# Optimization experiments

Hardware: AMD Instinct MI355X
Metric: run time of the kernel (lower is better)

## Reference

```python
import jax, jax.numpy as jnp
import numpy as np

CLASSES = 100
SIGMA = 1.0
K_MIX = 11   # mixup pseudo-label kNN
K_KNN = 3    # knn regularizer


def _pairwise_sq(a, b):
    # ||a_i - b_j||^2 via Gram trick; a:[M,D], b:[N,D] -> [M,N]
    aa = jnp.sum(a * a, axis=1)[:, None]
    bb = jnp.sum(b * b, axis=1)[None, :]
    return aa + bb - 2.0 * (a @ b.T)


def _mode_rows(vals):
    # vals: [M,K] float labels. torch.mode semantics: most frequent value,
    # smallest value on ties.
    eq = vals[:, :, None] == vals[:, None, :]      # [M,K,K]
    counts = jnp.sum(eq.astype(vals.dtype), axis=2)  # [M,K]
    maxc = jnp.max(counts, axis=1, keepdims=True)
    masked = jnp.where(counts == maxc, vals, jnp.inf)
    return jnp.min(masked, axis=1)


def setup_inputs() -> dict:
    key = jax.random.key(0)
    k1, k2, k3, k4 = jax.random.split(key, 4)
    N, D = 4096, 512
    x = jax.random.normal(k1, (N, D), dtype=jnp.float32)
    y = jax.random.randint(k2, (N,), 0, CLASSES).astype(jnp.float32)
    lam = jax.random.beta(k3, 2.0, 2.0, (), dtype=jnp.float32)  # Beta(alpha=2, alpha=2)
    perm = jax.random.permutation(k4, N).astype(jnp.int32)
    return {"x": x, "y": y, "lam": lam, "perm": perm}


def reference(x, y, lam, perm):
    # ---- mixup branch: pseudo-label mixed samples via k=11 NN mode ----
    x_ul = x * lam + x[perm] * (1.0 - lam)              # [N,D]
    d = _pairwise_sq(x_ul, x)                            # [N,N]
    _, idx = jax.lax.top_k(-d, K_MIX)                    # indices of k smallest dists
    y_ul = _mode_rows(y[idx])                            # [N]
    x = jnp.concatenate([x, x_ul], axis=0)               # [2N,D]
    y = jnp.concatenate([y, y_ul], axis=0)               # [2N]

    num = x.shape[0]
    y_int = y.astype(jnp.int32)
    # per-class means (empty classes masked out, as the torch loop skips them)
    counts = jax.ops.segment_sum(jnp.ones((num,), x.dtype), y_int, num_segments=CLASSES)
    mu = jax.ops.segment_sum(x, y_int, num_segments=CLASSES) / jnp.maximum(counts, 1.0)[:, None]
    d2 = _pairwise_sq(x, mu)                             # [num, classes]
    pi = jnp.exp(-d2 / (2.0 * SIGMA ** 2)) * (counts > 0).astype(x.dtype)[None, :]
    yh = jax.nn.one_hot(y_int, CLASSES, dtype=x.dtype)
    eps = 1e-15
    pi = pi / (jnp.sum(pi, axis=1, keepdims=True) + eps)
    pi = jnp.clip(pi, 0.0, 1.0)
    loss_gm = jnp.mean(jnp.sum((pi - yh) ** 2, axis=1))

    # ---- knn regularizer: k=3 NN (excluding self) mode label, MSE ----
    dk = _pairwise_sq(x, x)                              # [num,num]
    _, idxk = jax.lax.top_k(-dk, K_KNN + 1)              # nearest is self (dist 0)
    y_ng = _mode_rows(y[idxk[:, 1:]])
    loss_knn = jnp.mean((y_ng - y) ** 2)
    return loss_gm + 0.01 * loss_knn
```

## Files before the change

### kernel.cpp

```cpp
#include <hip/hip_runtime.h>
#include <math.h>

#define N0   4096
#define D    512
#define NUM  8192
#define NCLS 100
#define KMIX 11

#define OFF_NALL   0
#define OFF_YALL   8192
#define OFF_RLOSS  16384
#define OFF_KSQ    24576
#define OFF_MUSUM  32768
#define OFF_CNT    83968
#define OFF_KNN    84096
#define ZERO_N     51344
#define OFF_NMU    84112
#define OFF_MUT    84224
#define OFF_TK1S   135424
#define OFF_TK1I   659712
#define OFF_TK2S   1184000
#define OFF_TK2I   1446144
#define OFF_XH     1708288
#define TOTAL_F    3805440
#define NEED_BYTES ((size_t)TOTAL_F * 4)

typedef _Float16 half8 __attribute__((ext_vector_type(8)));
typedef _Float16 half4v __attribute__((ext_vector_type(4)));
typedef float f32x4 __attribute__((ext_vector_type(4)));
typedef unsigned long long u64;

__device__ __forceinline__ float4 ld_row4(const float* __restrict__ x, const int* __restrict__ perm,
                                          float lam, float om, int r, int col) {
  if (r < N0) {
    return *(const float4*)(x + (size_t)r * D + col);
  } else {
    int rr = r - N0;
    int p = perm[rr];
    float4 a = *(const float4*)(x + (size_t)rr * D + col);
    float4 b = *(const float4*)(x + (size_t)p * D + col);
    float4 m;
    m.x = lam * a.x + om * b.x;  m.y = lam * a.y + om * b.y;
    m.z = lam * a.z + om * b.z;  m.w = lam * a.w + om * b.w;
    return m;
  }
}

__device__ __forceinline__ void gld_lds16(const _Float16* g, _Float16* l) {
  __builtin_amdgcn_global_load_lds(
      (const __attribute__((address_space(1))) void*)g,
      (__attribute__((address_space(3))) void*)l, 16, 0, 0);
}

__device__ __forceinline__ unsigned sortable(float s) {
  unsigned u = __float_as_uint(s);
  return ((int)u < 0) ? ~u : (u | 0x80000000u);
}
__device__ __forceinline__ float unsortable(unsigned u) {
  return __uint_as_float(((int)u < 0) ? (u & 0x7fffffffu) : ~u);
}

__global__ __launch_bounds__(256) void k_zero(float* __restrict__ p, int n) {
  int i = blockIdx.x * 256 + threadIdx.x;
  if (i < n) p[i] = 0.f;
}

__global__ __launch_bounds__(256) void k_y(const float* __restrict__ y, float* __restrict__ y_all) {
  int i = blockIdx.x * 256 + threadIdx.x;
  if (i < N0) y_all[i] = y[i];
}

__global__ __launch_bounds__(64) void k_prep(const float* __restrict__ x, const float* __restrict__ y,
                                             const int* __restrict__ perm, const float* __restrict__ lam_p,
                                             _Float16* __restrict__ Xh, float* __restrict__ n_all,
                                             float* __restrict__ y_all) {
  int i = blockIdx.x;
  float lam = lam_p[0], om = 1.0f - lam;
  int t = threadIdx.x;
  float4 a = ld_row4(x, perm, lam, om, i, t * 4);
  float4 b = ld_row4(x, perm, lam, om, i, t * 4 + 256);
  half4v ha, hb;
  ha.x = (_Float16)a.x; ha.y = (_Float16)a.y; ha.z = (_Float16)a.z; ha.w = (_Float16)a.w;
  hb.x = (_Float16)b.x; hb.y = (_Float16)b.y; hb.z = (_Float16)b.z; hb.w = (_Float16)b.w;
  *(half4v*)(Xh + (size_t)i * D + t * 4) = ha;
  *(half4v*)(Xh + (size_t)i * D + t * 4 + 256) = hb;
  float s = a.x*a.x + a.y*a.y + a.z*a.z + a.w*a.w
          + b.x*b.x + b.y*b.y + b.z*b.z + b.w*b.w;
  #pragma unroll
  for (int o = 32; o > 0; o >>= 1) s += __shfl_down(s, o, 64);
  if (t == 0) {
    n_all[i] = s;
    if (i < N0) y_all[i] = y[i];
  }
}

template<int M, int NSPL>
__device__ __forceinline__ void knn_body(const _Float16* __restrict__ Xq,
                                         const _Float16* __restrict__ Xc,
                                         const float* __restrict__ nC,
                                         int cb0, int candPerSplit,
                                         int row0, int split,
                                         float* __restrict__ outS, int* __restrict__ outI,
                                         char* smem) {
  float* Ss = (float*)smem;
  _Float16* St = (_Float16*)smem;
  u64* Lb = (u64*)smem;

  int tid = threadIdx.x;
  int wave = tid >> 6, lane = tid & 63;
  int wq = wave >> 1, wc = wave & 1;
  int col16 = lane & 15, quad = lane >> 4;

  const _Float16* qg = Xq + (size_t)(wave * 16 + col16) * D + quad * 8;
  int csegA = 2 * wave, csegB = 2 * wave + 1;
  int ldsQ = wave * 1024 + lane * 8;
  int ldsCA = 4096 + csegA * 1024 + lane * 8;
  int ldsCB = 4096 + csegB * 1024 + lane * 8;

  u64 keys[M];
  #pragma unroll
  for (int q = 0; q < M; q++) keys[q] = ~0ULL;

  int r_scan = tid & 63, h_scan = tid >> 6;

  for (int c0 = 0; c0 < candPerSplit; c0 += 128) {
    const _Float16* cgA = Xc + (size_t)(cb0 + c0 + csegA * 16 + col16) * D + quad * 8;
    const _Float16* cgB = cgA + (size_t)16 * D;

    f32x4 acc[2][4];
    #pragma unroll
    for (int i = 0; i < 2; i++)
      #pragma unroll
      for (int j = 0; j < 4; j++) acc[i][j] = (f32x4){0.f, 0.f, 0.f, 0.f};

    gld_lds16(qg,       St + ldsQ);
    gld_lds16(qg + 32,  St + ldsQ + 512);
    gld_lds16(cgA,      St + ldsCA);
    gld_lds16(cgA + 32, St + ldsCA + 512);
    gld_lds16(cgB,      St + ldsCB);
    gld_lds16(cgB + 32, St + ldsCB + 512);
    __syncthreads();

    #pragma unroll
    for (int t = 0; t < 8; t++) {
      const int cur = t & 1;
      if (t < 7) {
        int kk = (t + 1) * 64;
        _Float16* B = St + (cur ^ 1) * 12288;
        gld_lds16(qg + kk,       B + ldsQ);
        gld_lds16(qg + kk + 32,  B + ldsQ + 512);
        gld_lds16(cgA + kk,      B + ldsCA);
        gld_lds16(cgA + kk + 32, B + ldsCA + 512);
        gld_lds16(cgB + kk,      B + ldsCB);
        gld_lds16(cgB + kk + 32, B + ldsCB + 512);
      }
      const _Float16* Bc = St + cur * 12288;
      half8 a[2][2], b[4][2];
      #pragma unroll
      for (int i = 0; i < 2; i++)
        #pragma unroll
        for (int h = 0; h < 2; h++)
          a[i][h] = *(const half8*)(Bc + (wq * 2 + i) * 1024 + h * 512 + lane * 8);
      #pragma unroll
      for (int j = 0; j < 4; j++)
        #pragma unroll
        for (int h = 0; h < 2; h++)
          b[j][h] = *(const half8*)(Bc + 4096 + (wc * 4 + j) * 1024 + h * 512 + lane * 8);
      #pragma unroll
      for (int h = 0; h < 2; h++)
        #pragma unroll
        for (int i = 0; i < 2; i++)
          #pragma unroll
          for (int j = 0; j < 4; j++)
            acc[i][j] = __builtin_amdgcn_mfma_f32_16x16x32_f16(a[i][h], b[j][h], acc[i][j], 0, 0, 0);
      __syncthreads();
    }

    #pragma unroll
    for (int j = 0; j < 4; j++) {
      int c_local = wc * 64 + j * 16 + col16;
      float ncv = nC[cb0 + c0 + c_local];
      #pragma unroll
      for (int i = 0; i < 2; i++) {
        float4 st;
        st.x = ncv - 2.f * acc[i][j][0];
        st.y = ncv - 2.f * acc[i][j][1];
        st.z = ncv - 2.f * acc[i][j][2];
        st.w = ncv - 2.f * acc[i][j][3];
        *(float4*)&Ss[(size_t)c_local * 68 + wq * 32 + i * 16 + quad * 4] = st;
      }
    }
    __syncthreads();

    for (int c = h_scan * 32; c < h_scan * 32 + 32; c++) {
      float s = Ss[c * 68 + r_scan];
      u64 key = ((u64)sortable(s) << 32) | (unsigned)(cb0 + c0 + c);
      if (key < keys[M - 1]) {
        keys[M - 1] = key;
        #pragma unroll
        for (int p = M - 1; p > 0; p--) {
          if (keys[p] < keys[p - 1]) { u64 tmp = keys[p]; keys[p] = keys[p - 1]; keys[p - 1] = tmp; }
        }
      }
    }
    __syncthreads();
  }

  #pragma unroll
  for (int q = 0; q < M; q++)
    Lb[((size_t)h_scan * 64 + r_scan) * M + q] = keys[q];
  __syncthreads();
  if (tid < 64) {
    int p0 = 0, p1 = 0, p2 = 0, p3 = 0;
    const u64* L0 = Lb + (size_t)(0 * 64 + tid) * M;
    const u64* L1 = Lb + (size_t)(1 * 64 + tid) * M;
    const u64* L2 = Lb + (size_t)(2 * 64 + tid) * M;
    const u64* L3 = Lb + (size_t)(3 * 64 + tid) * M;
    size_t off = (size_t)(row0 + tid) * ((size_t)NSPL * M) + (size_t)split * M;
    #pragma unroll
    for (int q = 0; q < M; q++) {
      u64 k0 = (p0 < M) ? L0[p0] : ~0ULL;
      u64 k1 = (p1 < M) ? L1[p1] : ~0ULL;
      u64 k2 = (p2 < M) ? L2[p2] : ~0ULL;
      u64 k3 = (p3 < M) ? L3[p3] : ~0ULL;
      u64 b01 = k0 < k1 ? k0 : k1;
      u64 b23 = k2 < k3 ? k2 : k3;
      u64 b = b01 < b23 ? b01 : b23;
      if (b == k0) p0++; else if (b == k1) p1++; else if (b == k2) p2++; else p3++;
      outS[off + q] = unsortable((unsigned)(b >> 32));
      outI[off + q] = (int)(unsigned)b;
    }
  }
}

__global__ __launch_bounds__(256, 3) void k_knn_all(const _Float16* __restrict__ Xh,
                                                    const float* __restrict__ n_all,
                                                    float* __restrict__ tk1s, int* __restrict__ tk1i,
                                                    float* __restrict__ tk2s, int* __restrict__ tk2i) {
  __shared__ __align__(16) char smem[49152];
  int bx = blockIdx.x;
  if (bx < 512) {
    int qblk = bx & 127, split = bx >> 7;
    knn_body<8, 4>(Xh + (size_t)(qblk * 64) * D, Xh, n_all,
                   split * 2048, 2048, qblk * 64, split, tk2s, tk2i, smem);
  } else {
    int b = bx - 512;
    int qblk = b & 63, split = b >> 6;
    knn_body<16, 8>(Xh + (size_t)(N0 + qblk * 64) * D, Xh, n_all,
                    split * 512, 512, qblk * 64, split, tk1s, tk1i, smem);
  }
}

__global__ __launch_bounds__(256) void k_rr1(const float* __restrict__ x, const int* __restrict__ perm,
                                             const float* __restrict__ lam_p,
                                             const float* __restrict__ tks, const int* __restrict__ tki,
                                             const float* __restrict__ n_all, const float* __restrict__ y,
                                             float* __restrict__ y_all) {
  __shared__ int sidx[16];
  __shared__ float sdot[16];
  int i = blockIdx.x;
  int t = threadIdx.x;
  float lam = lam_p[0], om = 1.f - lam;
  if (t == 0) {
    const float* sb = tks + (size_t)i * 128;
    const int* ib = tki + (size_t)i * 128;
    int p[8] = {0,0,0,0,0,0,0,0};
    for (int q = 0; q < 16; q++) {
      float bs = 3.0e38f; int bi = 0x7fffffff; int w = 0;
      #pragma unroll
      for (int li = 0; li < 8; li++) {
        if (p[li] < 16) {
          float s = sb[li * 16 + p[li]]; int id = ib[li * 16 + p[li]];
          if (s < bs || (s == bs && id < bi)) { bs = s; bi = id; w = li; }
        }
      }
      p[w]++;
      sidx[q] = bi;
    }
  }
  __syncthreads();
  int g = t >> 4, l16 = t & 15;
  int c = sidx[g];
  float dot = 0.f;
  for (int d0 = l16 * 4; d0 < D; d0 += 64) {
    float4 q4 = ld_row4(x, perm, lam, om, N0 + i, d0);
    float4 c4 = *(const float4*)(x + (size_t)c * D + d0);
    dot += q4.x*c4.x + q4.y*c4.y + q4.z*c4.z + q4.w*c4.w;
  }
  #pragma unroll
  for (int o = 8; o > 0; o >>= 1) dot += __shfl_down(dot, o, 16);
  if (l16 == 0) sdot[g] = n_all[c] - 2.f * dot;
  __syncthreads();
  if (t == 0) {
    float es[16]; int ei[16];
    for (int q = 0; q < 16; q++) { es[q] = sdot[q]; ei[q] = sidx[q]; }
    for (int a = 1; a < 16; a++) {
      float s = es[a]; int id = ei[a];
      int b = a - 1;
      while (b >= 0 && (es[b] > s || (es[b] == s && ei[b] > id))) {
        es[b + 1] = es[b]; ei[b + 1] = ei[b]; b--;
      }
      es[b + 1] = s; ei[b + 1] = id;
    }
    float lab[KMIX];
    for (int q = 0; q < KMIX; q++) lab[q] = y[ei[q]];
    float best = 3.0e38f; int bestc = 0;
    for (int q = 0; q < KMIX; q++) {
      int cnt = 0;
      for (int r = 0; r < KMIX; r++) cnt += (lab[r] == lab[q]) ? 1 : 0;
      if (cnt > bestc || (cnt == bestc && lab[q] < best)) { bestc = cnt; best = lab[q]; }
    }
    y_all[N0 + i] = best;
  }
}

__global__ __launch_bounds__(256) void k_rr2(const float* __restrict__ x, const int* __restrict__ perm,
                                             const float* __restrict__ lam_p,
                                             const float* __restrict__ tks, const int* __restrict__ tki,
                                             const float* __restrict__ n_all, const float* __restrict__ y_all,
                                             float* __restrict__ ksq) {
  __shared__ int sidx[8];
  __shared__ float sdot[8];
  int i = blockIdx.x;
  int t = threadIdx.x;
  float lam = lam_p[0], om = 1.f - lam;
  if (t == 0) {
    const float* sb = tks + (size_t)i * 32;
    const int* ib = tki + (size_t)i * 32;
    int p[4] = {0,0,0,0};
    for (int q = 0; q < 8; q++) {
      float bs = 3.0e38f; int bi = 0x7fffffff; int w = 0;
      #pragma unroll
      for (int li = 0; li < 4; li++) {
        if (p[li] < 8) {
          float s = sb[li * 8 + p[li]]; int id = ib[li * 8 + p[li]];
          if (s < bs || (s == bs && id < bi)) { bs = s; bi = id; w = li; }
        }
      }
      p[w]++;
      sidx[q] = bi;
    }
  }
  __syncthreads();
  int g = t >> 5, l32 = t & 31;
  int c = sidx[g];
  float dot = 0.f;
  for (int d0 = l32 * 4; d0 < D; d0 += 128) {
    float4 q4 = ld_row4(x, perm, lam, om, i, d0);
    float4 c4 = ld_row4(x, perm, lam, om, c, d0);
    dot += q4.x*c4.x + q4.y*c4.y + q4.z*c4.z + q4.w*c4.w;
  }
  #pragma unroll
  for (int o = 16; o > 0; o >>= 1) dot += __shfl_down(dot, o, 32);
  if (l32 == 0) sdot[g] = n_all[c] - 2.f * dot;
  __syncthreads();
  if (t == 0) {
    float es[8]; int ei[8];
    for (int q = 0; q < 8; q++) { es[q] = sdot[q]; ei[q] = sidx[q]; }
    for (int a = 1; a < 8; a++) {
      float s = es[a]; int id = ei[a];
      int b = a - 1;
      while (b >= 0 && (es[b] > s || (es[b] == s && ei[b] > id))) {
        es[b + 1] = es[b]; ei[b + 1] = ei[b]; b--;
      }
      es[b + 1] = s; ei[b + 1] = id;
    }
    float l1 = y_all[ei[1]], l2 = y_all[ei[2]], l3 = y_all[ei[3]];
    int c1 = 1 + (int)(l2 == l1) + (int)(l3 == l1);
    int c2 = 1 + (int)(l1 == l2) + (int)(l3 == l2);
    int c3 = 1 + (int)(l1 == l3) + (int)(l2 == l3);
    int mc = c1 > c2 ? c1 : c2; mc = mc > c3 ? mc : c3;
    float mv = 3.0e38f;
    if (c1 == mc) mv = fminf(mv, l1);
    if (c2 == mc) mv = fminf(mv, l2);
    if (c3 == mc) mv = fminf(mv, l3);
    float d = mv - y_all[i];
    ksq[i] = d * d;
  }
}

__global__ __launch_bounds__(256) void k_stats2h(const float* __restrict__ x, const int* __restrict__ perm,
                                                 const float* __restrict__ lam_p, const float* __restrict__ y_all,
                                                 _Float16* __restrict__ muH, float* __restrict__ nmu_pad,
                                                 float* __restrict__ counts) {
  __shared__ int cnt;
  __shared__ int lst[NUM];
  __shared__ int lstp[NUM];
  __shared__ float red[256];
  int c = blockIdx.x;
  int t = threadIdx.x;
  if (c >= NCLS) {
    for (int d = t; d < D; d += 256) muH[(size_t)c * D + d] = (_Float16)0.f;
    if (t == 0) { nmu_pad[c] = 0.f; counts[c] = 0.f; }
    return;
  }
  float lam = lam_p[0], om = 1.f - lam;
  float fc = (float)c;
  if (t == 0) cnt = 0;
  __syncthreads();
  for (int i = t; i < NUM; i += 256) {
    if (y_all[i] == fc) {
      int pos = atomicAdd(&cnt, 1);
      lst[pos] = i;
      lstp[pos] = (i >= N0) ? perm[i - N0] : 0;
    }
  }
  __syncthreads();
  int n = cnt;
  float a0 = 0.f, a1 = 0.f;
  for (int m = 0; m < n; m++) {
    int i = lst[m];
    if (i < N0) {
      a0 += x[(size_t)i * D + t];
      a1 += x[(size_t)i * D + t + 256];
    } else {
      int rr = i - N0, p = lstp[m];
      a0 += lam * x[(size_t)rr * D + t] + om * x[(size_t)p * D + t];
      a1 += lam * x[(size_t)rr * D + t + 256] + om * x[(size_t)p * D + t + 256];
    }
  }
  float inv = 1.f / fmaxf((float)n, 1.f);
  float v0 = a0 * inv, v1 = a1 * inv;
  muH[(size_t)c * D + t] = (_Float16)v0;
  muH[(size_t)c * D + t + 256] = (_Float16)v1;
  red[t] = v0 * v0 + v1 * v1;
  __syncthreads();
  for (int o = 128; o > 0; o >>= 1) { if (t < o) red[t] += red[t + o]; __syncthreads(); }
  if (t == 0) { nmu_pad[c] = red[0]; counts[c] = (float)n; }
}

__global__ __launch_bounds__(256) void k_gm2(const _Float16* __restrict__ Xh,
                                             const _Float16* __restrict__ muH,
                                             const float* __restrict__ nmu_pad,
                                             const float* __restrict__ counts,
                                             const float* __restrict__ n_all,
                                             const float* __restrict__ y_all,
                                             float* __restrict__ rloss) {
  __shared__ __align__(16) char smem[49152];
  float* Ss = (float*)smem;
  _Float16* St = (_Float16*)smem;

  int tid = threadIdx.x;
  int wave = tid >> 6, lane = tid & 63;
  int wq = wave >> 1, wc = wave & 1;
  int col16 = lane & 15, quad = lane >> 4;
  int qb = blockIdx.x * 64;

  const _Float16* qg = Xh + (size_t)(qb + wave * 16 + col16) * D + quad * 8;
  int csegA = 2 * wave, csegB = 2 * wave + 1;
  const _Float16* cgA = muH + (size_t)(csegA * 16 + col16) * D + quad * 8;
  const _Float16* cgB = cgA + (size_t)16 * D;
  int ldsQ = wave * 1024 + lane * 8;
  int ldsCA = 4096 + csegA * 1024 + lane * 8;
  int ldsCB = 4096 + csegB * 1024 + lane * 8;

  f32x4 acc[2][4];
  #pragma unroll
  for (int i = 0; i < 2; i++)
    #pragma unroll
    for (int j = 0; j < 4; j++) acc[i][j] = (f32x4){0.f, 0.f, 0.f, 0.f};

  gld_lds16(qg,       St + ldsQ);
  gld_lds16(qg + 32,  St + ldsQ + 512);
  gld_lds16(cgA,      St + ldsCA);
  gld_lds16(cgA + 32, St + ldsCA + 512);
  gld_lds16(cgB,      St + ldsCB);
  gld_lds16(cgB + 32, St + ldsCB + 512);
  __syncthreads();

  #pragma unroll
  for (int t = 0; t < 8; t++) {
    const int cur = t & 1;
    if (t < 7) {
      int kk = (t + 1) * 64;
      _Float16* B = St + (cur ^ 1) * 12288;
      gld_lds16(qg + kk,       B + ldsQ);
      gld_lds16(qg + kk + 32,  B + ldsQ + 512);
      gld_lds16(cgA + kk,      B + ldsCA);
      gld_lds16(cgA + kk + 32, B + ldsCA + 512);
      gld_lds16(cgB + kk,      B + ldsCB);
      gld_lds16(cgB + kk + 32, B + ldsCB + 512);
    }
    const _Float16* Bc = St + cur * 12288;
    half8 a[2][2], b[4][2];
    #pragma unroll
    for (int i = 0; i < 2; i++)
      #pragma unroll
      for (int h = 0; h < 2; h++)
        a[i][h] = *(const half8*)(Bc + (wq * 2 + i) * 1024 + h * 512 + lane * 8);
    #pragma unroll
    for (int j = 0; j < 4; j++)
      #pragma unroll
      for (int h = 0; h < 2; h++)
        b[j][h] = *(const half8*)(Bc + 4096 + (wc * 4 + j) * 1024 + h * 512 + lane * 8);
// ... 214 lines not shown
    int c = 0;
    #pragma unroll
    for (int r = 0; r < KMIX; r++) c += (lab[r] == lab[q]) ? 1 : 0;
    if (c > bestc || (c == bestc && lab[q] < best)) { bestc = c; best = lab[q]; }
  }
  y_all[N0 + i] = best;
}

__global__ __launch_bounds__(128) void k_stats(const float* __restrict__ x, const int* __restrict__ perm,
                                               const float* __restrict__ lam_p, const float* __restrict__ y_all,
                                               float* __restrict__ mu_sum, float* __restrict__ counts) {
  int i = blockIdx.x;
  float lam = lam_p[0], om = 1.0f - lam;
  int c = (int)y_all[i];
  float* ms = mu_sum + (size_t)c * D;
  int t = threadIdx.x;
  float4 v = ld_row4(x, perm, lam, om, i, t * 4);
  atomicAdd(&ms[t * 4 + 0], v.x);
  atomicAdd(&ms[t * 4 + 1], v.y);
  atomicAdd(&ms[t * 4 + 2], v.z);
  atomicAdd(&ms[t * 4 + 3], v.w);
  if (t == 0) atomicAdd(&counts[c], 1.0f);
}

__global__ __launch_bounds__(256) void k_mufin(const float* __restrict__ mu_sum, const float* __restrict__ counts,
                                               float* __restrict__ muT, float* __restrict__ nmu) {
  __shared__ float red[256];
  int c = blockIdx.x;
  float inv = 1.0f / fmaxf(counts[c], 1.0f);
  int t = threadIdx.x;
  float v0 = mu_sum[(size_t)c * D + t] * inv;
  float v1 = mu_sum[(size_t)c * D + t + 256] * inv;
  muT[(size_t)t * NCLS + c] = v0;
  muT[(size_t)(t + 256) * NCLS + c] = v1;
  red[t] = v0 * v0 + v1 * v1;
  __syncthreads();
  for (int o = 128; o > 0; o >>= 1) { if (t < o) red[t] += red[t + o]; __syncthreads(); }
  if (t == 0) nmu[c] = red[0];
}

__global__ __launch_bounds__(256) void k_final2(const float* __restrict__ t2s, const int* __restrict__ t2i,
                                                const float* __restrict__ y_all, float* __restrict__ knn_acc) {
  __shared__ float red[256];
  int i = blockIdx.x * 256 + threadIdx.x;
  float dd2 = 0.f;
  if (i < NUM) {
    const float* sA = t2s + (size_t)i * 8; const float* sB = sA + 4;
    const int* iA = t2i + (size_t)i * 8;   const int* iB = iA + 4;
    int pa = 0, pb = 0;
    int midx[4];
    #pragma unroll
    for (int q = 0; q < 4; q++) {
      float sa = (pa < 4) ? sA[pa] : 3.0e38f;
      float sb = (pb < 4) ? sB[pb] : 3.0e38f;
      int ia = (pa < 4) ? iA[pa] : 0x7fffffff;
      int ib = (pb < 4) ? iB[pb] : 0x7fffffff;
      bool ta = (sa < sb) || (sa == sb && ia < ib);
      midx[q] = ta ? ia : ib;
      if (ta) pa++; else pb++;
    }
    float l1 = y_all[midx[1]], l2 = y_all[midx[2]], l3 = y_all[midx[3]];
    int c1 = 1 + (int)(l2 == l1) + (int)(l3 == l1);
    int c2 = 1 + (int)(l1 == l2) + (int)(l3 == l2);
    int c3 = 1 + (int)(l1 == l3) + (int)(l2 == l3);
    int mc = c1 > c2 ? c1 : c2; mc = mc > c3 ? mc : c3;
    float mv = 3.0e38f;
    if (c1 == mc) mv = fminf(mv, l1);
    if (c2 == mc) mv = fminf(mv, l2);
    if (c3 == mc) mv = fminf(mv, l3);
    float d = mv - y_all[i];
    dd2 = d * d;
  }
  red[threadIdx.x] = dd2;
  __syncthreads();
  for (int o = 128; o > 0; o >>= 1) { if (threadIdx.x < o) red[threadIdx.x] += red[threadIdx.x + o]; __syncthreads(); }
  if (threadIdx.x == 0) atomicAdd(knn_acc, red[0]);
}

__global__ __launch_bounds__(128) void k_gm(const float* __restrict__ x, const int* __restrict__ perm,
                                            const float* __restrict__ lam_p, const float* __restrict__ y_all,
                                            const float* __restrict__ n_all, const float* __restrict__ muT,
                                            const float* __restrict__ nmu, const float* __restrict__ counts,
                                            float* __restrict__ row_loss) {
  __shared__ float red[128];
  int i = blockIdx.x;
  int t = threadIdx.x;
  float lam = lam_p[0], om = 1.0f - lam;
  bool valid = (t < NCLS) && (counts[t] > 0.f);
  float d2 = 3.0e38f;
  if (t < NCLS) {
    float dot = 0.f;
    for (int d = 0; d < D; d += 4) {
      float4 v = ld_row4(x, perm, lam, om, i, d);
      dot += v.x * muT[(size_t)(d + 0) * NCLS + t];
      dot += v.y * muT[(size_t)(d + 1) * NCLS + t];
      dot += v.z * muT[(size_t)(d + 2) * NCLS + t];
      dot += v.w * muT[(size_t)(d + 3) * NCLS + t];
    }
    d2 = n_all[i] + nmu[t] - 2.f * dot;
  }
  red[t] = valid ? d2 : 3.0e38f;
  __syncthreads();
  for (int o = 64; o > 0; o >>= 1) { if (t < o) red[t] = fminf(red[t], red[t + o]); __syncthreads(); }
  float m = red[0];
  __syncthreads();
  float e = valid ? expf(-0.5f * (d2 - m)) : 0.f;
  red[t] = e;
  __syncthreads();
  for (int o = 64; o > 0; o >>= 1) { if (t < o) red[t] += red[t + o]; __syncthreads(); }
  float S = red[0];
  __syncthreads();
  float E = expf(-0.5f * m);
  float denom = E * S + 1e-15f;
  float pi = e * E / denom;
  pi = fminf(fmaxf(pi, 0.f), 1.f);
  int yc = (int)y_all[i];
  float term = pi * pi - 2.f * ((t == yc) ? pi : 0.f);
  red[t] = valid ? term : 0.f;
  __syncthreads();
  for (int o = 64; o > 0; o >>= 1) { if (t < o) red[t] += red[t + o]; __syncthreads(); }
  if (t == 0) row_loss[i] = red[0] + 1.0f;
}

__global__ __launch_bounds__(256) void k_final_slow(const float* __restrict__ row_loss,
                                                    const float* __restrict__ knn_acc, float* __restrict__ out) {
  __shared__ float red[256];
  int t = threadIdx.x;
  float s = 0.f;
  for (int i = t; i < NUM; i += 256) s += row_loss[i];
  red[t] = s;
  __syncthreads();
  for (int o = 128; o > 0; o >>= 1) { if (t < o) red[t] += red[t + o]; __syncthreads(); }
  if (t == 0) out[0] = red[0] / (float)NUM + 0.01f * (knn_acc[0] / (float)NUM);
}

extern "C" void kernel_launch(void* const* d_in, const int* in_sizes, int n_in,
                              void* d_out, int out_size, void* d_ws, size_t ws_size,
                              hipStream_t stream) {
  const float* x   = (const float*)d_in[0];
  const float* y   = (const float*)d_in[1];
  const float* lam = (const float*)d_in[2];
  const int* perm  = (const int*)d_in[3];
  float* ws = (float*)d_ws;

  float* n_all  = ws + OFF_NALL;
  float* y_all  = ws + OFF_YALL;
  float* rloss  = ws + OFF_RLOSS;
  float* ksq    = ws + OFF_KSQ;
  float* mu_sum = ws + OFF_MUSUM;
  float* counts = ws + OFF_CNT;
  float* knn_acc= ws + OFF_KNN;
  float* nmu    = ws + OFF_NMU;
  float* muT    = ws + OFF_MUT;
  float* tk1s   = ws + OFF_TK1S;
  int*   tk1i   = (int*)(ws + OFF_TK1I);
  float* tk2s   = ws + OFF_TK2S;
  int*   tk2i   = (int*)(ws + OFF_TK2I);
  _Float16* Xh  = (_Float16*)(ws + OFF_XH);
  _Float16* muH = (_Float16*)(ws + OFF_MUSUM);
  float* nmu_pad= ws + OFF_MUT;

  bool fast = ws_size >= NEED_BYTES;

  if (fast) {
    k_prep<<<NUM, 64, 0, stream>>>(x, y, perm, lam, Xh, n_all, y_all);
    k_knn_all<<<1024, 256, 0, stream>>>(Xh, n_all, tk1s, tk1i, tk2s, tk2i);
    k_rr1<<<N0, 256, 0, stream>>>(x, perm, lam, tk1s, tk1i, n_all, y, y_all);
    k_stats2h<<<128, 256, 0, stream>>>(x, perm, lam, y_all, muH, nmu_pad, counts);
    k_rr2<<<NUM, 256, 0, stream>>>(x, perm, lam, tk2s, tk2i, n_all, y_all, ksq);
    k_gm2<<<NUM / 64, 256, 0, stream>>>(Xh, muH, nmu_pad, counts, n_all, y_all, rloss);
    k_final_fast<<<1, 256, 0, stream>>>(rloss, ksq, (float*)d_out);
  } else {
    k_y<<<(N0 + 255) / 256, 256, 0, stream>>>(y, y_all);
    k_zero<<<(ZERO_N + 255) / 256, 256, 0, stream>>>(mu_sum, ZERO_N);
    k_norms<<<NUM, 64, 0, stream>>>(x, perm, lam, n_all);
    dim3 g1(N0 / QT, 4);
    k_knn_f32<KMIX><<<g1, 256, 0, stream>>>(x, perm, lam, N0, n_all, N0 / 4, 4, tk1s, tk1i);
    k_final1<<<(N0 + 255) / 256, 256, 0, stream>>>(tk1s, tk1i, y, y_all);
    k_stats<<<NUM, 128, 0, stream>>>(x, perm, lam, y_all, mu_sum, counts);
    k_mufin<<<NCLS, 256, 0, stream>>>(mu_sum, counts, muT, nmu);
    dim3 g2(NUM / QT, 2);
    k_knn_f32<4><<<g2, 256, 0, stream>>>(x, perm, lam, 0, n_all, NUM / 2, 2, tk2s, tk2i);
    k_final2<<<NUM / 256, 256, 0, stream>>>(tk2s, tk2i, y_all, knn_acc);
    k_gm<<<NUM, 128, 0, stream>>>(x, perm, lam, y_all, n_all, muT, nmu, counts, rloss);
    k_final_slow<<<1, 256, 0, stream>>>(rloss, knn_acc, (float*)d_out);
  }
}
```

Baseline: 699.1 us.

## Enlarge kNN query tile to 128 rows, store scores as fp16, parallelize candidate merges

The kNN kernel now processes 128 queries per block instead of 64, giving each wave a 64x64 MFMA tile. This halves how often candidate tiles are reloaded per query and reduces the number of splits and the grid size. Distance scores are staged in LDS as fp16, which saves shared memory and lets the scan use two threads per row. The rerank kernels replace the serial single-thread merge of split candidates with a parallel rank-based selection. Risks are lower occupancy (2 blocks per CU, 64KB LDS), less parallelism from the smaller grid, and fp16 rounding of scores possibly changing neighbor ordering before the fp32 rerank.

```diff
diff --git a/kernel.cpp b/kernel.cpp
--- a/kernel.cpp
+++ b/kernel.cpp
@@ -18,12 +18,15 @@
 #define OFF_NMU    84112
 #define OFF_MUT    84224
 #define OFF_TK1S   135424
-#define OFF_TK1I   659712
-#define OFF_TK2S   1184000
-#define OFF_TK2I   1446144
-#define OFF_XH     1708288
-#define TOTAL_F    3805440
-#define NEED_BYTES ((size_t)TOTAL_F * 4)
+#define OFF_TK1I   266496
+#define OFF_TK2S   397568
+#define OFF_TK2I   921856
+#define OFF_XH     1446144
+#define SOFF_TK1S  135424
+#define SOFF_TK1I  315648
+#define SOFF_TK2S  495872
+#define SOFF_TK2I  561408
+#define NEED_BYTES ((size_t)15221760)
 
 typedef _Float16 half8 __attribute__((ext_vector_type(8)));
 typedef _Float16 half4v __attribute__((ext_vector_type(4)));
@@ -95,15 +98,13 @@
 }
 
 template<int M, int NSPL>
-__device__ __forceinline__ void knn_body(const _Float16* __restrict__ Xq,
-                                         const _Float16* __restrict__ Xc,
-                                         const float* __restrict__ nC,
-                                         int cb0, int candPerSplit,
-                                         int row0, int split,
-                                         float* __restrict__ outS, int* __restrict__ outI,
-                                         char* smem) {
-  float* Ss = (float*)smem;
+__device__ __forceinline__ void knn_body128(
+    const _Float16* __restrict__ Xq, const _Float16* __restrict__ Xc,
+    const float* __restrict__ nC, int cb0, int nctiles, int row0, int split,
+    float* __restrict__ outS, int* __restrict__ outI, char* smem)
+{
   _Float16* St = (_Float16*)smem;
+  _Float16* Sh = (_Float16*)smem;
   u64* Lb = (u64*)smem;
 
   int tid = threadIdx.x;
@@ -111,34 +112,34 @@
   int wq = wave >> 1, wc = wave & 1;
   int col16 = lane & 15, quad = lane >> 4;
 
-  const _Float16* qg = Xq + (size_t)(wave * 16 + col16) * D + quad * 8;
-  int csegA = 2 * wave, csegB = 2 * wave + 1;
-  int ldsQ = wave * 1024 + lane * 8;
-  int ldsCA = 4096 + csegA * 1024 + lane * 8;
-  int ldsCB = 4096 + csegB * 1024 + lane * 8;
+  const _Float16* qA = Xq + (size_t)((2 * wave) * 16 + col16) * D + quad * 8;
+  const _Float16* qB = qA + (size_t)16 * D;
+  int lQA = (2 * wave) * 1024 + lane * 8;
+  int lQB = lQA + 1024;
+  int lCA = 8192 + (2 * wave) * 1024 + lane * 8;
+  int lCB = lCA + 1024;
 
   u64 keys[M];
   #pragma unroll
   for (int q = 0; q < M; q++) keys[q] = ~0ULL;
 
-  int r_scan = tid & 63, h_scan = tid >> 6;
-
-  for (int c0 = 0; c0 < candPerSplit; c0 += 128) {
-    const _Float16* cgA = Xc + (size_t)(cb0 + c0 + csegA * 16 + col16) * D + quad * 8;
-    const _Float16* cgB = cgA + (size_t)16 * D;
-
-    f32x4 acc[2][4];
-    #pragma unroll
-    for (int i = 0; i < 2; i++)
+  int r_scan = tid >> 1, h_scan = tid & 1;
+
+  for (int ct = 0; ct < nctiles; ct++) {
+    int c0 = cb0 + ct * 128;
+    const _Float16* cA = Xc + (size_t)(c0 + (2 * wave) * 16 + col16) * D + quad * 8;
+    const _Float16* cB = cA + (size_t)16 * D;
+
+    f32x4 acc[4][4];
+    #pragma unroll
+    for (int i = 0; i < 4; i++)
       #pragma unroll
       for (int j = 0; j < 4; j++) acc[i][j] = (f32x4){0.f, 0.f, 0.f, 0.f};
 
-    gld_lds16(qg,       St + ldsQ);
-    gld_lds16(qg + 32,  St + ldsQ + 512);
-    gld_lds16(cgA,      St + ldsCA);
-    gld_lds16(cgA + 32, St + ldsCA + 512);
-    gld_lds16(cgB,      St + ldsCB);
-    gld_lds16(cgB + 32, St + ldsCB + 512);
+    gld_lds16(qA,      St + lQA); gld_lds16(qA + 32, St + lQA + 512);
+    gld_lds16(qB,      St + lQB); gld_lds16(qB + 32, St + lQB + 512);
+    gld_lds16(cA,      St + lCA); gld_lds16(cA + 32, St + lCA + 512);
+    gld_lds16(cB,      St + lCB); gld_lds16(cB + 32, St + lCB + 512);
     __syncthreads();
 
     #pragma unroll
@@ -146,30 +147,28 @@
       const int cur = t & 1;
       if (t < 7) {
         int kk = (t + 1) * 64;
-        _Float16* B = St + (cur ^ 1) * 12288;
-        gld_lds16(qg + kk,       B + ldsQ);
-        gld_lds16(qg + kk + 32,  B + ldsQ + 512);
-        gld_lds16(cgA + kk,      B + ldsCA);
-        gld_lds16(cgA + kk + 32, B + ldsCA + 512);
-        gld_lds16(cgB + kk,      B + ldsCB);
-        gld_lds16(cgB + kk + 32, B + ldsCB + 512);
+        _Float16* B = St + (cur ^ 1) * 16384;
+        gld_lds16(qA + kk,      B + lQA); gld_lds16(qA + kk + 32, B + lQA + 512);
+        gld_lds16(qB + kk,      B + lQB); gld_lds16(qB + kk + 32, B + lQB + 512);
+        gld_lds16(cA + kk,      B + lCA); gld_lds16(cA + kk + 32, B + lCA + 512);
+        gld_lds16(cB + kk,      B + lCB); gld_lds16(cB + kk + 32, B + lCB + 512);
       }
-      const _Float16* Bc = St + cur * 12288;
-      half8 a[2][2], b[4][2];
-      #pragma unroll
-      for (int i = 0; i < 2; i++)
+      const _Float16* Bc = St + cur * 16384;
+      half8 a[4][2], b[4][2];
+      #pragma unroll
+      for (int i = 0; i < 4; i++)
         #pragma unroll
         for (int h = 0; h < 2; h++)
-          a[i][h] = *(const half8*)(Bc + (wq * 2 + i) * 1024 + h * 512 + lane * 8);
+          a[i][h] = *(const half8*)(Bc + (wq * 4 + i) * 1024 + h * 512 + lane * 8);
       #pragma unroll
       for (int j = 0; j < 4; j++)
         #pragma unroll
         for (int h = 0; h < 2; h++)
-          b[j][h] = *(const half8*)(Bc + 4096 + (wc * 4 + j) * 1024 + h * 512 + lane * 8);
+          b[j][h] = *(const half8*)(Bc + 8192 + (wc * 4 + j) * 1024 + h * 512 + lane * 8);
       #pragma unroll
       for (int h = 0; h < 2; h++)
         #pragma unroll
-        for (int i = 0; i < 2; i++)
+        for (int i = 0; i < 4; i++)
           #pragma unroll
           for (int j = 0; j < 4; j++)
             acc[i][j] = __builtin_amdgcn_mfma_f32_16x16x32_f16(a[i][h], b[j][h], acc[i][j], 0, 0, 0);
@@ -178,23 +177,23 @@
 
     #pragma unroll
     for (int j = 0; j < 4; j++) {
-      int c_local = wc * 64 + j * 16 + col16;
-      float ncv = nC[cb0 + c0 + c_local];
-      #pragma unroll
-      for (int i = 0; i < 2; i++) {
-        float4 st;
-        st.x = ncv - 2.f * acc[i][j][0];
-        st.y = ncv - 2.f * acc[i][j][1];
-        st.z = ncv - 2.f * acc[i][j][2];
-        st.w = ncv - 2.f * acc[i][j][3];
-        *(float4*)&Ss[(size_t)c_local * 68 + wq * 32 + i * 16 + quad * 4] = st;
+      int cl = wc * 64 + j * 16 + col16;
+      float ncv = nC[c0 + cl];
+      #pragma unroll
+      for (int i = 0; i < 4; i++) {
+        half4v st;
+        st.x = (_Float16)(ncv - 2.f * acc[i][j][0]);
+        st.y = (_Float16)(ncv - 2.f * acc[i][j][1]);
+        st.z = (_Float16)(ncv - 2.f * acc[i][j][2]);
+        st.w = (_Float16)(ncv - 2.f * acc[i][j][3]);
+        *(half4v*)&Sh[(size_t)cl * 132 + wq * 64 + i * 16 + quad * 4] = st;
       }
     }
     __syncthreads();
 
-    for (int c = h_scan * 32; c < h_scan * 32 + 32; c++) {
-      float s = Ss[c * 68 + r_scan];
-      u64 key = ((u64)sortable(s) << 32) | (unsigned)(cb0 + c0 + c);
+    for (int c = h_scan * 64; c < h_scan * 64 + 64; c++) {
+      float s = (float)Sh[c * 132 + r_scan];
+      u64 key = ((u64)sortable(s) << 32) | (unsigned)(c0 + c);
       if (key < keys[M - 1]) {
         keys[M - 1] = key;
         #pragma unroll
@@ -208,46 +207,40 @@
 
   #pragma unroll
   for (int q = 0; q < M; q++)
-    Lb[((size_t)h_scan * 64 + r_scan) * M + q] = keys[q];
-  __syncthreads();
-  if (tid < 64) {
-    int p0 = 0, p1 = 0, p2 = 0, p3 = 0;
-    const u64* L0 = Lb + (size_t)(0 * 64 + tid) * M;
-    const u64* L1 = Lb + (size_t)(1 * 64 + tid) * M;
-    const u64* L2 = Lb + (size_t)(2 * 64 + tid) * M;
-    const u64* L3 = Lb + (size_t)(3 * 64 + tid) * M;
+    Lb[((size_t)h_scan * 128 + r_scan) * M + q] = keys[q];
+  __syncthreads();
+  if (tid < 128) {
+    const u64* L0 = Lb + (size_t)tid * M;
+    const u64* L1 = Lb + (size_t)(128 + tid) * M;
+    int p0 = 0, p1 = 0;
     size_t off = (size_t)(row0 + tid) * ((size_t)NSPL * M) + (size_t)split * M;
     #pragma unroll
     for (int q = 0; q < M; q++) {
       u64 k0 = (p0 < M) ? L0[p0] : ~0ULL;
       u64 k1 = (p1 < M) ? L1[p1] : ~0ULL;
-      u64 k2 = (p2 < M) ? L2[p2] : ~0ULL;
-      u64 k3 = (p3 < M) ? L3[p3] : ~0ULL;
-      u64 b01 = k0 < k1 ? k0 : k1;
-      u64 b23 = k2 < k3 ? k2 : k3;
-      u64 b = b01 < b23 ? b01 : b23;
-      if (b == k0) p0++; else if (b == k1) p1++; else if (b == k2) p2++; else p3++;
+      u64 b = k0 < k1 ? k0 : k1;
+      if (b == k0) p0++; else p1++;
       outS[off + q] = unsortable((unsigned)(b >> 32));
       outI[off + q] = (int)(unsigned)b;
     }
   }
 }
 
-__global__ __launch_bounds__(256, 3) void k_knn_all(const _Float16* __restrict__ Xh,
+__global__ __launch_bounds__(256, 2) void k_knn_all(const _Float16* __restrict__ Xh,
                                                     const float* __restrict__ n_all,
                                                     float* __restrict__ tk1s, int* __restrict__ tk1i,
                                                     float* __restrict__ tk2s, int* __restrict__ tk2i) {
-  __shared__ __align__(16) char smem[49152];
+  __shared__ __align__(16) char smem[65536];
   int bx = blockIdx.x;
-  if (bx < 512) {
-    int qblk = bx & 127, split = bx >> 7;
-    knn_body<8, 4>(Xh + (size_t)(qblk * 64) * D, Xh, n_all,
-                   split * 2048, 2048, qblk * 64, split, tk2s, tk2i, smem);
+  if (bx < 64) {
+    int qblk = bx & 31, split = bx >> 5;
+    knn_body128<16, 2>(Xh + (size_t)(N0 + qblk * 128) * D, Xh, n_all,
+                       split * 2048, 16, qblk * 128, split, tk1s, tk1i, smem);
   } else {
-    int b = bx - 512;
+    int b = bx - 64;
     int qblk = b & 63, split = b >> 6;
-    knn_body<16, 8>(Xh + (size_t)(N0 + qblk * 64) * D, Xh, n_all,
-                    split * 512, 512, qblk * 64, split, tk1s, tk1i, smem);
+    knn_body128<8, 8>(Xh + (size_t)(qblk * 128) * D, Xh, n_all,
+                      split * 1024, 8, qblk * 128, split, tk2s, tk2i, smem);
   }
 }
 
@@ -256,27 +249,24 @@
                                              const float* __restrict__ tks, const int* __restrict__ tki,
                                              const float* __restrict__ n_all, const float* __restrict__ y,
                                              float* __restrict__ y_all) {
+  __shared__ u64 kl[32];
   __shared__ int sidx[16];
   __shared__ float sdot[16];
   int i = blockIdx.x;
   int t = threadIdx.x;
   float lam = lam_p[0], om = 1.f - lam;
-  if (t == 0) {
-    const float* sb = tks + (size_t)i * 128;
-    const int* ib = tki + (size_t)i * 128;
-    int p[8] = {0,0,0,0,0,0,0,0};
-    for (int q = 0; q < 16; q++) {
-      float bs = 3.0e38f; int bi = 0x7fffffff; int w = 0;
-      #pragma unroll
-      for (int li = 0; li < 8; li++) {
-        if (p[li] < 16) {
-          float s = sb[li * 16 + p[li]]; int id = ib[li * 16 + p[li]];
-          if (s < bs || (s == bs && id < bi)) { bs = s; bi = id; w = li; }
-        }
-      }
-      p[w]++;
-      sidx[q] = bi;
-    }
+  if (t < 32) {
+    float s = tks[(size_t)i * 32 + t];
+    int id = tki[(size_t)i * 32 + t];
+    kl[t] = ((u64)sortable(s) << 32) | (unsigned)id;
+  }
+  __syncthreads();
+  if (t < 32) {
+    u64 me = kl[t];
+    int rank = 0;
+    #pragma unroll
+    for (int j = 0; j < 32; j++) rank += (kl[j] < me) ? 1 : 0;
+    if (rank < 16) sidx[rank] = (int)(unsigned)me;
   }
   __syncthreads();
   int g = t >> 4, l16 = t & 15;
@@ -319,27 +309,24 @@
                                              const float* __restrict__ tks, const int* __restrict__ tki,
                                              const float* __restrict__ n_all, const float* __restrict__ y_all,
                                              float* __restrict__ ksq) {
+  __shared__ u64 kl[64];
   __shared__ int sidx[8];
   __shared__ float sdot[8];
   int i = blockIdx.x;
   int t = threadIdx.x;
   float lam = lam_p[0], om = 1.f - lam;
-  if (t == 0) {
-    const float* sb = tks + (size_t)i * 32;
-    const int* ib = tki + (size_t)i * 32;
-    int p[4] = {0,0,0,0};
-    for (int q = 0; q < 8; q++) {
-      float bs = 3.0e38f; int bi = 0x7fffffff; int w = 0;
-      #pragma unroll
-      for (int li = 0; li < 4; li++) {
-        if (p[li] < 8) {
-          float s = sb[li * 8 + p[li]]; int id = ib[li * 8 + p[li]];
-          if (s < bs || (s == bs && id < bi)) { bs = s; bi = id; w = li; }
-        }
-      }
-      p[w]++;
-      sidx[q] = bi;
-    }
+  if (t < 64) {
+    float s = tks[(size_t)i * 64 + t];
+    int id = tki[(size_t)i * 64 + t];
+    kl[t] = ((u64)sortable(s) << 32) | (unsigned)id;
+  }
+  __syncthreads();
+  if (t < 64) {
+    u64 me = kl[t];
+    int rank = 0;
+    #pragma unroll
+    for (int j = 0; j < 64; j++) rank += (kl[j] < me) ? 1 : 0;
+    if (rank < 8) sidx[rank] = (int)(unsigned)me;
   }
   __syncthreads();
   int g = t >> 5, l32 = t & 31;
@@ -860,10 +847,6 @@
   float* knn_acc= ws + OFF_KNN;
   float* nmu    = ws + OFF_NMU;
   float* muT    = ws + OFF_MUT;
-  float* tk1s   = ws + OFF_TK1S;
-  int*   tk1i   = (int*)(ws + OFF_TK1I);
-  float* tk2s   = ws + OFF_TK2S;
-  int*   tk2i   = (int*)(ws + OFF_TK2I);
   _Float16* Xh  = (_Float16*)(ws + OFF_XH);
   _Float16* muH = (_Float16*)(ws + OFF_MUSUM);
   float* nmu_pad= ws + OFF_MUT;
@@ -871,14 +854,18 @@
   bool fast = ws_size >= NEED_BYTES;
 
   if (fast) {
+    float* tk1s = ws + OFF_TK1S;  int* tk1i = (int*)(ws + OFF_TK1I);
+    float* tk2s = ws + OFF_TK2S;  int* tk2i = (int*)(ws + OFF_TK2I);
     k_prep<<<NUM, 64, 0, stream>>>(x, y, perm, lam, Xh, n_all, y_all);
-    k_knn_all<<<1024, 256, 0, stream>>>(Xh, n_all, tk1s, tk1i, tk2s, tk2i);
+    k_knn_all<<<576, 256, 0, stream>>>(Xh, n_all, tk1s, tk1i, tk2s, tk2i);
     k_rr1<<<N0, 256, 0, stream>>>(x, perm, lam, tk1s, tk1i, n_all, y, y_all);
     k_stats2h<<<128, 256, 0, stream>>>(x, perm, lam, y_all, muH, nmu_pad, counts);
     k_rr2<<<NUM, 256, 0, stream>>>(x, perm, lam, tk2s, tk2i, n_all, y_all, ksq);
     k_gm2<<<NUM / 64, 256, 0, stream>>>(Xh, muH, nmu_pad, counts, n_all, y_all, rloss);
     k_final_fast<<<1, 256, 0, stream>>>(rloss, ksq, (float*)d_out);
   } else {
+    float* tk1s = ws + SOFF_TK1S;  int* tk1i = (int*)(ws + SOFF_TK1I);
+    float* tk2s = ws + SOFF_TK2S;  int* tk2i = (int*)(ws + SOFF_TK2I);
     k_y<<<(N0 + 255) / 256, 256, 0, stream>>>(y, y_all);
     k_zero<<<(ZERO_N + 255) / 256, 256, 0, stream>>>(mu_sum, ZERO_N);
     k_norms<<<NUM, 64, 0, stream>>>(x, perm, lam, n_all);
```

Result: slower. 935.1 us (+33.7%).

## Prefetch next candidate tile across iterations, store scores as fp16, parallelize merge

Applied to the files above, without the earlier changes.

The kNN kernel now issues the first k-slice of the next candidate tile during the last k-step of the current tile. This removes the separate load-and-sync prologue that ran at the start of every tile. The score staging buffer is moved to its own LDS region and stored as fp16, so it no longer aliases the double buffer being prefetched and uses half the space. The rerank kernels replace the serial one-thread k-way merge with a parallel rank count over all candidate keys. The cost is reduced precision in the candidate scores used for top-k selection, which may change which candidates are kept.

```diff
diff --git a/kernel.cpp b/kernel.cpp
--- a/kernel.cpp
+++ b/kernel.cpp
@@ -98,12 +98,11 @@
 __device__ __forceinline__ void knn_body(const _Float16* __restrict__ Xq,
                                          const _Float16* __restrict__ Xc,
                                          const float* __restrict__ nC,
-                                         int cb0, int candPerSplit,
-                                         int row0, int split,
+                                         int cb0, int nctiles, int row0, int split,
                                          float* __restrict__ outS, int* __restrict__ outI,
                                          char* smem) {
-  float* Ss = (float*)smem;
   _Float16* St = (_Float16*)smem;
+  _Float16* Sh = (_Float16*)(smem + 24576);
   u64* Lb = (u64*)smem;
 
   int tid = threadIdx.x;
@@ -123,8 +122,18 @@
 
   int r_scan = tid & 63, h_scan = tid >> 6;
 
-  for (int c0 = 0; c0 < candPerSplit; c0 += 128) {
-    const _Float16* cgA = Xc + (size_t)(cb0 + c0 + csegA * 16 + col16) * D + quad * 8;
+  {
+    const _Float16* cA = Xc + (size_t)(cb0 + csegA * 16 + col16) * D + quad * 8;
+    const _Float16* cB = cA + (size_t)16 * D;
+    gld_lds16(qg,      St + ldsQ);  gld_lds16(qg + 32, St + ldsQ + 512);
+    gld_lds16(cA,      St + ldsCA); gld_lds16(cA + 32, St + ldsCA + 512);
+    gld_lds16(cB,      St + ldsCB); gld_lds16(cB + 32, St + ldsCB + 512);
+  }
+  __syncthreads();
+
+  for (int ct = 0; ct < nctiles; ct++) {
+    int c0 = cb0 + ct * 128;
+    const _Float16* cgA = Xc + (size_t)(c0 + csegA * 16 + col16) * D + quad * 8;
     const _Float16* cgB = cgA + (size_t)16 * D;
 
     f32x4 acc[2][4];
@@ -132,14 +141,6 @@
     for (int i = 0; i < 2; i++)
       #pragma unroll
       for (int j = 0; j < 4; j++) acc[i][j] = (f32x4){0.f, 0.f, 0.f, 0.f};
-
-    gld_lds16(qg,       St + ldsQ);
-    gld_lds16(qg + 32,  St + ldsQ + 512);
-    gld_lds16(cgA,      St + ldsCA);
-    gld_lds16(cgA + 32, St + ldsCA + 512);
-    gld_lds16(cgB,      St + ldsCB);
-    gld_lds16(cgB + 32, St + ldsCB + 512);
-    __syncthreads();
 
     #pragma unroll
     for (int t = 0; t < 8; t++) {
@@ -147,12 +148,15 @@
       if (t < 7) {
         int kk = (t + 1) * 64;
         _Float16* B = St + (cur ^ 1) * 12288;
-        gld_lds16(qg + kk,       B + ldsQ);
-        gld_lds16(qg + kk + 32,  B + ldsQ + 512);
-        gld_lds16(cgA + kk,      B + ldsCA);
-        gld_lds16(cgA + kk + 32, B + ldsCA + 512);
-        gld_lds16(cgB + kk,      B + ldsCB);
-        gld_lds16(cgB + kk + 32, B + ldsCB + 512);
+        gld_lds16(qg + kk,       B + ldsQ);  gld_lds16(qg + kk + 32,  B + ldsQ + 512);
+        gld_lds16(cgA + kk,      B + ldsCA); gld_lds16(cgA + kk + 32, B + ldsCA + 512);
+        gld_lds16(cgB + kk,      B + ldsCB); gld_lds16(cgB + kk + 32, B + ldsCB + 512);
+      } else if (ct + 1 < nctiles) {
+        const _Float16* nA = cgA + (size_t)128 * D;
+        const _Float16* nB = cgB + (size_t)128 * D;
+        gld_lds16(qg,      St + ldsQ);  gld_lds16(qg + 32, St + ldsQ + 512);
+        gld_lds16(nA,      St + ldsCA); gld_lds16(nA + 32, St + ldsCA + 512);
+        gld_lds16(nB,      St + ldsCB); gld_lds16(nB + 32, St + ldsCB + 512);
       }
       const _Float16* Bc = St + cur * 12288;
       half8 a[2][2], b[4][2];
@@ -178,23 +182,23 @@
 
     #pragma unroll
     for (int j = 0; j < 4; j++) {
-      int c_local = wc * 64 + j * 16 + col16;
-      float ncv = nC[cb0 + c0 + c_local];
+      int cl = wc * 64 + j * 16 + col16;
+      float ncv = nC[c0 + cl];
       #pragma unroll
       for (int i = 0; i < 2; i++) {
-        float4 st;
-        st.x = ncv - 2.f * acc[i][j][0];
-        st.y = ncv - 2.f * acc[i][j][1];
-        st.z = ncv - 2.f * acc[i][j][2];
-        st.w = ncv - 2.f * acc[i][j][3];
-        *(float4*)&Ss[(size_t)c_local * 68 + wq * 32 + i * 16 + quad * 4] = st;
+        half4v st;
+        st.x = (_Float16)(ncv - 2.f * acc[i][j][0]);
+        st.y = (_Float16)(ncv - 2.f * acc[i][j][1]);
+        st.z = (_Float16)(ncv - 2.f * acc[i][j][2]);
+        st.w = (_Float16)(ncv - 2.f * acc[i][j][3]);
+        *(half4v*)&Sh[(size_t)cl * 68 + wq * 32 + i * 16 + quad * 4] = st;
       }
     }
     __syncthreads();
 
     for (int c = h_scan * 32; c < h_scan * 32 + 32; c++) {
-      float s = Ss[c * 68 + r_scan];
-      u64 key = ((u64)sortable(s) << 32) | (unsigned)(cb0 + c0 + c);
+      float s = (float)Sh[c * 68 + r_scan];
+      u64 key = ((u64)sortable(s) << 32) | (unsigned)(c0 + c);
       if (key < keys[M - 1]) {
         keys[M - 1] = key;
         #pragma unroll
@@ -242,12 +246,12 @@
   if (bx < 512) {
     int qblk = bx & 127, split = bx >> 7;
     knn_body<8, 4>(Xh + (size_t)(qblk * 64) * D, Xh, n_all,
-                   split * 2048, 2048, qblk * 64, split, tk2s, tk2i, smem);
+                   split * 2048, 16, qblk * 64, split, tk2s, tk2i, smem);
   } else {
     int b = bx - 512;
     int qblk = b & 63, split = b >> 6;
     knn_body<16, 8>(Xh + (size_t)(N0 + qblk * 64) * D, Xh, n_all,
-                    split * 512, 512, qblk * 64, split, tk1s, tk1i, smem);
+                    split * 512, 4, qblk * 64, split, tk1s, tk1i, smem);
   }
 }
 
@@ -256,27 +260,23 @@
                                              const float* __restrict__ tks, const int* __restrict__ tki,
                                              const float* __restrict__ n_all, const float* __restrict__ y,
                                              float* __restrict__ y_all) {
+  __shared__ u64 kl[128];
   __shared__ int sidx[16];
   __shared__ float sdot[16];
   int i = blockIdx.x;
   int t = threadIdx.x;
   float lam = lam_p[0], om = 1.f - lam;
-  if (t == 0) {
-    const float* sb = tks + (size_t)i * 128;
-    const int* ib = tki + (size_t)i * 128;
-    int p[8] = {0,0,0,0,0,0,0,0};
-    for (int q = 0; q < 16; q++) {
-      float bs = 3.0e38f; int bi = 0x7fffffff; int w = 0;
-      #pragma unroll
-      for (int li = 0; li < 8; li++) {
-        if (p[li] < 16) {
-          float s = sb[li * 16 + p[li]]; int id = ib[li * 16 + p[li]];
-          if (s < bs || (s == bs && id < bi)) { bs = s; bi = id; w = li; }
-        }
-      }
-      p[w]++;
-      sidx[q] = bi;
-    }
+  if (t < 128) {
+    float s = tks[(size_t)i * 128 + t];
+    int id = tki[(size_t)i * 128 + t];
+    kl[t] = ((u64)sortable(s) << 32) | (unsigned)id;
+  }
+  __syncthreads();
+  if (t < 128) {
+    u64 me = kl[t];
+    int rank = 0;
+    for (int j = 0; j < 128; j++) rank += (kl[j] < me) ? 1 : 0;
+    if (rank < 16) sidx[rank] = (int)(unsigned)me;
   }
   __syncthreads();
   int g = t >> 4, l16 = t & 15;
@@ -319,27 +319,24 @@
                                              const float* __restrict__ tks, const int* __restrict__ tki,
                                              const float* __restrict__ n_all, const float* __restrict__ y_all,
                                              float* __restrict__ ksq) {
+  __shared__ u64 kl[32];
   __shared__ int sidx[8];
   __shared__ float sdot[8];
   int i = blockIdx.x;
   int t = threadIdx.x;
   float lam = lam_p[0], om = 1.f - lam;
-  if (t == 0) {
-    const float* sb = tks + (size_t)i * 32;
-    const int* ib = tki + (size_t)i * 32;
-    int p[4] = {0,0,0,0};
-    for (int q = 0; q < 8; q++) {
-      float bs = 3.0e38f; int bi = 0x7fffffff; int w = 0;
-      #pragma unroll
-      for (int li = 0; li < 4; li++) {
-        if (p[li] < 8) {
-          float s = sb[li * 8 + p[li]]; int id = ib[li * 8 + p[li]];
-          if (s < bs || (s == bs && id < bi)) { bs = s; bi = id; w = li; }
-        }
-      }
-      p[w]++;
-      sidx[q] = bi;
-    }
+  if (t < 32) {
+    float s = tks[(size_t)i * 32 + t];
+    int id = tki[(size_t)i * 32 + t];
+    kl[t] = ((u64)sortable(s) << 32) | (unsigned)id;
+  }
+  __syncthreads();
+  if (t < 32) {
+    u64 me = kl[t];
+    int rank = 0;
+    #pragma unroll
+    for (int j = 0; j < 32; j++) rank += (kl[j] < me) ? 1 : 0;
+    if (rank < 8) sidx[rank] = (int)(unsigned)me;
   }
   __syncthreads();
   int g = t >> 5, l32 = t & 31;
```

After: 633.5 us (median of 2 runs). -9.4%, faster.
